# Performance work log

Hardware: AMD Instinct MI355X
Metric: run time of the kernel (lower is better)

Reference implementation:

```python
import jax, jax.numpy as jnp
import numpy as np

BS, H, S, D = 2, 16, 4096, 64
BLOCK = 64
STRIDE_C = 3
NEG = -10000.0


def _global_index(seq_len, block_size, stride_c):
    # static Longformer-style global pattern: first token of each block plus
    # the last `stride_c` tokens of each block
    r = np.arange(seq_len)
    rem = r % block_size
    return np.nonzero((rem == 0) | (rem >= block_size - stride_c))[0]


def setup_inputs() -> dict:
    key = jax.random.key(0)
    k1, k2, k3 = jax.random.split(key, 3)
    q = jax.random.normal(k1, (BS, H, S, D), dtype=jnp.float32)
    k = jax.random.normal(k2, (BS, H, S, D), dtype=jnp.float32)
    v = jax.random.normal(k3, (BS, H, S, D), dtype=jnp.float32)
    mask = jnp.ones((BS, S), dtype=jnp.float32)  # all tokens valid -> pattern is static
    return {"query": q, "key": k, "value": v, "mask": mask}


def reference(query, key, value, mask):
    bs, h, S, d = query.shape
    block = BLOCK
    nb = S // block  # seq_len chosen as multiple of block_size, so pad_len == 0
    g_idx = jnp.asarray(_global_index(S, block, STRIDE_C))  # [G]

    # ---- block-local attention scores ----
    bq = query.reshape(bs, h, nb, block, d)
    bk = key.reshape(bs, h, nb, block, d)
    local = jnp.einsum('bhnxd,bhnyd->bhnxy', bq, bk)  # [bs,h,nb,block,block]
    # additive key-side mask (per key position within each block)
    key_mask = jnp.where(mask == 0.0, NEG, 0.0).reshape(bs, 1, nb, 1, block)
    local = (local + key_mask).reshape(bs, h, S, block)

    # ---- global-token attention scores ----
    gk = key[:, :, g_idx, :]    # [bs,h,G,d]
    gv = value[:, :, g_idx, :]  # [bs,h,G,d]
    gscores = jnp.einsum('bhsd,bhgd->bhsg', query, gk)  # [bs,h,S,G]
    gmask = jnp.where(mask[:, g_idx] == 0.0, NEG, 0.0)[:, None, None, :]
    gscores = gscores + gmask

    # ---- joint softmax over [local block | global tokens] ----
    scores = jnp.concatenate([local, gscores], axis=-1)  # [bs,h,S,block+G]
    probs = jax.nn.softmax(scores.astype(jnp.float32), axis=-1)

    # ---- weighted sums ----
    lp = probs[..., :block].reshape(bs, h, nb, block, block)
    bv = value.reshape(bs, h, nb, block, d)
    lout = jnp.matmul(lp, bv).reshape(bs, h, S, d)
    gout = jnp.einsum('bhsg,bhgd->bhsd', probs[..., block:], gv)
    return lout + gout
```

## Files before the change

kernel.cpp:

```cpp
#include <hip/hip_runtime.h>

#define NEGV -10000.0f

typedef _Float16 f16x8 __attribute__((ext_vector_type(8)));
typedef _Float16 f16x2 __attribute__((ext_vector_type(2)));
typedef float floatx4 __attribute__((ext_vector_type(4)));

__device__ __forceinline__ int src_row(int key, int nblk) {
    if (key < 64) return nblk * 64 + key;
    int g = key - 64;
    int p = g & 3;
    return (g >> 2) * 64 + (p ? (60 + p) : 0);
}

__global__ __launch_bounds__(256, 3)
void sparse_attn_kernel(const float* __restrict__ Q, const float* __restrict__ K,
                        const float* __restrict__ V, const float* __restrict__ M,
                        float* __restrict__ O)
{
    const int x    = blockIdx.x;
    const int bh   = (x & 7) * 4 + ((x >> 3) >> 6);
    const int nblk = (x >> 3) & 63;
    const int b    = bh >> 4;

    const size_t hoff = (size_t)bh * (4096 * 64);
    const float* Qh = Q + hoff;
    const float* Kh = K + hoff;
    const float* Vh = V + hoff;
    float*       Oh = O + hoff;
    const float* Mb = M + (size_t)b * 4096;

    __shared__ _Float16 smem[20480];

    const int tid  = threadIdx.x;
    const int lane = tid & 63;
    const int wv   = tid >> 6;
    const int m    = lane & 15;
    const int quad = lane >> 4;
    const int cg   = tid & 15;
    const int pg   = tid >> 4;

    float mv2[5];
    unsigned long long bb = 0ull;
    #pragma unroll
    for (int s = 0; s < 5; ++s) {
        float mval = Mb[src_row(s * 64 + lane, nblk)];
        bb |= __ballot(mval == 0.0f);
        mv2[s] = (mval == 0.0f) ? NEGV : 0.0f;
    }

    const int qrow = nblk * 64 + wv * 16 + m;
    f16x8 qf[2];
    #pragma unroll
    for (int c = 0; c < 2; ++c) {
        const float* src = Qh + (size_t)qrow * 64 + c * 32 + quad * 8;
        float4 f0 = *(const float4*)src;
        float4 f1 = *(const float4*)(src + 4);
        qf[c][0] = (_Float16)f0.x; qf[c][1] = (_Float16)f0.y;
        qf[c][2] = (_Float16)f0.z; qf[c][3] = (_Float16)f0.w;
        qf[c][4] = (_Float16)f1.x; qf[c][5] = (_Float16)f1.y;
        qf[c][6] = (_Float16)f1.z; qf[c][7] = (_Float16)f1.w;
    }

    #pragma unroll
    for (int it = 0; it < 10; ++it) {
        int S    = it * 256 + tid;
        int t    = S >> 7;
        int n    = S & 15;
        int col0 = ((S >> 6) & 1) * 32 + ((S & 63) >> 4) * 8;
        int lkey = 32 * (t >> 1) + 8 * (n >> 2) + 4 * (t & 1) + (n & 3);
        const float* src = Kh + (size_t)src_row(lkey, nblk) * 64 + col0;
        float4 f0 = *(const float4*)src;
        float4 f1 = *(const float4*)(src + 4);
        f16x8 o;
        o[0] = (_Float16)f0.x; o[1] = (_Float16)f0.y;
        o[2] = (_Float16)f0.z; o[3] = (_Float16)f0.w;
        o[4] = (_Float16)f1.x; o[5] = (_Float16)f1.y;
        o[6] = (_Float16)f1.z; o[7] = (_Float16)f1.w;
        *(f16x8*)(&smem[S * 8]) = o;
    }

    float4 v0a[5], v0b[5];
    #pragma unroll
    for (int it = 0; it < 5; ++it) {
        int l0 = 2 * (it * 16 + pg);
        v0a[it] = *(const float4*)(Vh + (size_t)src_row(l0,     nblk) * 64 + cg * 4);
        v0b[it] = *(const float4*)(Vh + (size_t)src_row(l0 + 1, nblk) * 64 + cg * 4);
    }

    __syncthreads();

    floatx4 acc[20] = {};
    #pragma unroll
    for (int t = 0; t < 20; ++t) {
        #pragma unroll
        for (int c = 0; c < 2; ++c) {
            f16x8 kf = *(const f16x8*)(&smem[(t * 2 + c) * 512 + lane * 8]);
            acc[t] = __builtin_amdgcn_mfma_f32_16x16x32_f16(kf, qf[c], acc[t], 0, 0, 0);
        }
    }

    __syncthreads();

    auto vt_store = [&](int l0, const float4& f0, const float4& f1) {
        int kc2   = l0 >> 5;
        int q2    = (l0 & 31) >> 3;
        int j0    = l0 & 7;
        int td    = cg >> 2;
        int sw    = td << 4;
        int lbase = (kc2 * 4 + td) * 512 + q2 * 128 + (cg & 3) * 32 + j0;
        f16x2 pk0; pk0[0] = (_Float16)f0.x; pk0[1] = (_Float16)f1.x;
        *(f16x2*)(&smem[(lbase +  0) ^ sw]) = pk0;
        f16x2 pk1; pk1[0] = (_Float16)f0.y; pk1[1] = (_Float16)f1.y;
        *(f16x2*)(&smem[(lbase +  8) ^ sw]) = pk1;
        f16x2 pk2; pk2[0] = (_Float16)f0.z; pk2[1] = (_Float16)f1.z;
        *(f16x2*)(&smem[(lbase + 16) ^ sw]) = pk2;
        f16x2 pk3; pk3[0] = (_Float16)f0.w; pk3[1] = (_Float16)f1.w;
        *(f16x2*)(&smem[(lbase + 24) ^ sw]) = pk3;
    };

    #pragma unroll
    for (int it = 0; it < 5; ++it)
        vt_store(2 * (it * 16 + pg), v0a[it], v0b[it]);

    float4 v1a[5], v1b[5];
    #pragma unroll
    for (int it = 0; it < 5; ++it) {
        int l0 = 2 * ((5 + it) * 16 + pg);
        v1a[it] = *(const float4*)(Vh + (size_t)src_row(l0,     nblk) * 64 + cg * 4);
        v1b[it] = *(const float4*)(Vh + (size_t)src_row(l0 + 1, nblk) * 64 + cg * 4);
    }

    if (bb != 0ull) {
        #pragma unroll
        for (int t = 0; t < 20; ++t) {
            int lb = 32 * ((t >> 1) & 1) + 4 * (t & 1) + 8 * quad;
            #pragma unroll
            for (int r = 0; r < 4; ++r)
                acc[t][r] += __shfl(mv2[t >> 2], lb + r, 64);
        }
    }

    float rmax = -3e38f;
    #pragma unroll
    for (int t = 0; t < 20; ++t)
        #pragma unroll
        for (int r = 0; r < 4; ++r)
            rmax = fmaxf(rmax, acc[t][r]);
    rmax = fmaxf(rmax, __shfl_xor(rmax, 16, 64));
    rmax = fmaxf(rmax, __shfl_xor(rmax, 32, 64));
    float rsum = 0.f;
    #pragma unroll
    for (int t = 0; t < 20; ++t)
        #pragma unroll
        for (int r = 0; r < 4; ++r) {
            float e = __expf(acc[t][r] - rmax);
            acc[t][r] = e;
            rsum += e;
        }
    rsum += __shfl_xor(rsum, 16, 64);
    rsum += __shfl_xor(rsum, 32, 64);
    float rinv = 1.0f / rsum;

    #pragma unroll
    for (int it = 0; it < 5; ++it)
        vt_store(2 * ((5 + it) * 16 + pg), v1a[it], v1b[it]);

    f16x8 pf[10];
    #pragma unroll
    for (int k2 = 0; k2 < 10; ++k2) {
        #pragma unroll
        for (int r = 0; r < 4; ++r) {
            pf[k2][r]     = (_Float16)acc[2 * k2][r];
            pf[k2][4 + r] = (_Float16)acc[2 * k2 + 1][r];
        }
    }

    __syncthreads();

    floatx4 oacc[4] = {};
    #pragma unroll
    for (int k2 = 0; k2 < 10; ++k2) {
        #pragma unroll
        for (int t = 0; t < 4; ++t) {
            f16x8 vf = *(const f16x8*)(&smem[(k2 * 4 + t) * 512 + ((lane * 8) ^ (t << 4))]);
            oacc[t] = __builtin_amdgcn_mfma_f32_16x16x32_f16(pf[k2], vf, oacc[t], 0, 0, 0);
        }
    }

    float rinvr[4];
    #pragma unroll
    for (int r = 0; r < 4; ++r)
        rinvr[r] = __shfl(rinv, quad * 4 + r, 64);
    #pragma unroll
    for (int t = 0; t < 4; ++t)
        #pragma unroll
        for (int r = 0; r < 4; ++r)
            Oh[(size_t)(nblk * 64 + wv * 16 + quad * 4 + r) * 64 + t * 16 + m] =
                oacc[t][r] * rinvr[r];
}

extern "C" void kernel_launch(void* const* d_in, const int* in_sizes, int n_in,
                              void* d_out, int out_size, void* d_ws, size_t ws_size,
                              hipStream_t stream) {
    const float* q    = (const float*)d_in[0];
    const float* k    = (const float*)d_in[1];
    const float* v    = (const float*)d_in[2];
    const float* mask = (const float*)d_in[3];
    float* out = (float*)d_out;
    (void)in_sizes; (void)n_in; (void)out_size; (void)d_ws; (void)ws_size;
    sparse_attn_kernel<<<2 * 16 * 64, 256, 0, stream>>>(q, k, v, mask, out);
}
```

Before: 156.8 us.

## Stage V loads in smaller batches to raise occupancy to four blocks per CU

```diff
diff --git a/kernel.cpp b/kernel.cpp
--- a/kernel.cpp
+++ b/kernel.cpp
@@ -13,7 +13,7 @@
     return (g >> 2) * 64 + (p ? (60 + p) : 0);
 }
 
-__global__ __launch_bounds__(256, 3)
+__global__ __launch_bounds__(256, 4)
 void sparse_attn_kernel(const float* __restrict__ Q, const float* __restrict__ K,
                         const float* __restrict__ V, const float* __restrict__ M,
                         float* __restrict__ O)
@@ -80,29 +80,13 @@
         *(f16x8*)(&smem[S * 8]) = o;
     }
 
-    float4 v0a[5], v0b[5];
-    #pragma unroll
-    for (int it = 0; it < 5; ++it) {
+    auto v_load = [&](int it, float4& f0, float4& f1) {
         int l0 = 2 * (it * 16 + pg);
-        v0a[it] = *(const float4*)(Vh + (size_t)src_row(l0,     nblk) * 64 + cg * 4);
-        v0b[it] = *(const float4*)(Vh + (size_t)src_row(l0 + 1, nblk) * 64 + cg * 4);
-    }
-
-    __syncthreads();
-
-    floatx4 acc[20] = {};
-    #pragma unroll
-    for (int t = 0; t < 20; ++t) {
-        #pragma unroll
-        for (int c = 0; c < 2; ++c) {
-            f16x8 kf = *(const f16x8*)(&smem[(t * 2 + c) * 512 + lane * 8]);
-            acc[t] = __builtin_amdgcn_mfma_f32_16x16x32_f16(kf, qf[c], acc[t], 0, 0, 0);
-        }
-    }
-
-    __syncthreads();
-
-    auto vt_store = [&](int l0, const float4& f0, const float4& f1) {
+        f0 = *(const float4*)(Vh + (size_t)src_row(l0,     nblk) * 64 + cg * 4);
+        f1 = *(const float4*)(Vh + (size_t)src_row(l0 + 1, nblk) * 64 + cg * 4);
+    };
+    auto vt_store = [&](int it, const float4& f0, const float4& f1) {
+        int l0    = 2 * (it * 16 + pg);
         int kc2   = l0 >> 5;
         int q2    = (l0 & 31) >> 3;
         int j0    = l0 & 7;
@@ -119,17 +103,32 @@
         *(f16x2*)(&smem[(lbase + 24) ^ sw]) = pk3;
     };
 
-    #pragma unroll
-    for (int it = 0; it < 5; ++it)
-        vt_store(2 * (it * 16 + pg), v0a[it], v0b[it]);
-
-    float4 v1a[5], v1b[5];
-    #pragma unroll
-    for (int it = 0; it < 5; ++it) {
-        int l0 = 2 * ((5 + it) * 16 + pg);
-        v1a[it] = *(const float4*)(Vh + (size_t)src_row(l0,     nblk) * 64 + cg * 4);
-        v1b[it] = *(const float4*)(Vh + (size_t)src_row(l0 + 1, nblk) * 64 + cg * 4);
-    }
+    float4 va0, vb0, va1, vb1, va2, vb2;
+    v_load(0, va0, vb0);
+    v_load(1, va1, vb1);
+    v_load(2, va2, vb2);
+
+    __syncthreads();
+
+    floatx4 acc[20] = {};
+    #pragma unroll
+    for (int t = 0; t < 20; ++t) {
+        #pragma unroll
+        for (int c = 0; c < 2; ++c) {
+            f16x8 kf = *(const f16x8*)(&smem[(t * 2 + c) * 512 + lane * 8]);
+            acc[t] = __builtin_amdgcn_mfma_f32_16x16x32_f16(kf, qf[c], acc[t], 0, 0, 0);
+        }
+    }
+
+    __syncthreads();
+
+    float4 wa0, wb0, wa1, wb1, wa2, wb2;
+    v_load(3, wa0, wb0);
+    v_load(4, wa1, wb1);
+    v_load(5, wa2, wb2);
+    vt_store(0, va0, vb0);
+    vt_store(1, va1, vb1);
+    vt_store(2, va2, vb2);
 
     if (bb != 0ull) {
         #pragma unroll
@@ -149,6 +148,11 @@
             rmax = fmaxf(rmax, acc[t][r]);
     rmax = fmaxf(rmax, __shfl_xor(rmax, 16, 64));
     rmax = fmaxf(rmax, __shfl_xor(rmax, 32, 64));
+
+    vt_store(3, wa0, wb0);
+    vt_store(4, wa1, wb1);
+    vt_store(5, wa2, wb2);
+
     float rsum = 0.f;
     #pragma unroll
     for (int t = 0; t < 20; ++t)
@@ -162,9 +166,9 @@
     rsum += __shfl_xor(rsum, 32, 64);
     float rinv = 1.0f / rsum;
 
-    #pragma unroll
-    for (int it = 0; it < 5; ++it)
-        vt_store(2 * ((5 + it) * 16 + pg), v1a[it], v1b[it]);
+    v_load(6, va0, vb0);
+    v_load(7, va1, vb1);
+    v_load(8, va2, vb2);
 
     f16x8 pf[10];
     #pragma unroll
@@ -175,6 +179,12 @@
             pf[k2][4 + r] = (_Float16)acc[2 * k2 + 1][r];
         }
     }
+
+    vt_store(6, va0, vb0);
+    vt_store(7, va1, vb1);
+    vt_store(8, va2, vb2);
+    v_load(9, wa0, wb0);
+    vt_store(9, wa0, wb0);
 
     __syncthreads();
 
```

New measurement: 170.5 us. +8.8%, slower.

## Load K fragments directly from global into registers, skipping LDS staging

Applied to the files above, without the earlier changes.

```diff
diff --git a/kernel.cpp b/kernel.cpp
--- a/kernel.cpp
+++ b/kernel.cpp
@@ -11,6 +11,15 @@
     int g = key - 64;
     int p = g & 3;
     return (g >> 2) * 64 + (p ? (60 + p) : 0);
+}
+
+__device__ __forceinline__ f16x8 cvt8(const float4& f0, const float4& f1) {
+    f16x8 o;
+    o[0] = (_Float16)f0.x; o[1] = (_Float16)f0.y;
+    o[2] = (_Float16)f0.z; o[3] = (_Float16)f0.w;
+    o[4] = (_Float16)f1.x; o[5] = (_Float16)f1.y;
+    o[6] = (_Float16)f1.z; o[7] = (_Float16)f1.w;
+    return o;
 }
 
 __global__ __launch_bounds__(256, 3)
@@ -56,53 +65,16 @@
         const float* src = Qh + (size_t)qrow * 64 + c * 32 + quad * 8;
         float4 f0 = *(const float4*)src;
         float4 f1 = *(const float4*)(src + 4);
-        qf[c][0] = (_Float16)f0.x; qf[c][1] = (_Float16)f0.y;
-        qf[c][2] = (_Float16)f0.z; qf[c][3] = (_Float16)f0.w;
-        qf[c][4] = (_Float16)f1.x; qf[c][5] = (_Float16)f1.y;
-        qf[c][6] = (_Float16)f1.z; qf[c][7] = (_Float16)f1.w;
-    }
-
-    #pragma unroll
-    for (int it = 0; it < 10; ++it) {
-        int S    = it * 256 + tid;
-        int t    = S >> 7;
-        int n    = S & 15;
-        int col0 = ((S >> 6) & 1) * 32 + ((S & 63) >> 4) * 8;
-        int lkey = 32 * (t >> 1) + 8 * (n >> 2) + 4 * (t & 1) + (n & 3);
-        const float* src = Kh + (size_t)src_row(lkey, nblk) * 64 + col0;
-        float4 f0 = *(const float4*)src;
-        float4 f1 = *(const float4*)(src + 4);
-        f16x8 o;
-        o[0] = (_Float16)f0.x; o[1] = (_Float16)f0.y;
-        o[2] = (_Float16)f0.z; o[3] = (_Float16)f0.w;
-        o[4] = (_Float16)f1.x; o[5] = (_Float16)f1.y;
-        o[6] = (_Float16)f1.z; o[7] = (_Float16)f1.w;
-        *(f16x8*)(&smem[S * 8]) = o;
-    }
-
-    float4 v0a[5], v0b[5];
-    #pragma unroll
-    for (int it = 0; it < 5; ++it) {
+        qf[c] = cvt8(f0, f1);
+    }
+
+    auto v_load = [&](int it, float4& f0, float4& f1) {
         int l0 = 2 * (it * 16 + pg);
-        v0a[it] = *(const float4*)(Vh + (size_t)src_row(l0,     nblk) * 64 + cg * 4);
-        v0b[it] = *(const float4*)(Vh + (size_t)src_row(l0 + 1, nblk) * 64 + cg * 4);
-    }
-
-    __syncthreads();
-
-    floatx4 acc[20] = {};
-    #pragma unroll
-    for (int t = 0; t < 20; ++t) {
-        #pragma unroll
-        for (int c = 0; c < 2; ++c) {
-            f16x8 kf = *(const f16x8*)(&smem[(t * 2 + c) * 512 + lane * 8]);
-            acc[t] = __builtin_amdgcn_mfma_f32_16x16x32_f16(kf, qf[c], acc[t], 0, 0, 0);
-        }
-    }
-
-    __syncthreads();
-
-    auto vt_store = [&](int l0, const float4& f0, const float4& f1) {
+        f0 = *(const float4*)(Vh + (size_t)src_row(l0,     nblk) * 64 + cg * 4);
+        f1 = *(const float4*)(Vh + (size_t)src_row(l0 + 1, nblk) * 64 + cg * 4);
+    };
+    auto vt_store = [&](int it, const float4& f0, const float4& f1) {
+        int l0    = 2 * (it * 16 + pg);
         int kc2   = l0 >> 5;
         int q2    = (l0 & 31) >> 3;
         int j0    = l0 & 7;
@@ -119,17 +91,33 @@
         *(f16x2*)(&smem[(lbase + 24) ^ sw]) = pk3;
     };
 
-    #pragma unroll
-    for (int it = 0; it < 5; ++it)
-        vt_store(2 * (it * 16 + pg), v0a[it], v0b[it]);
-
-    float4 v1a[5], v1b[5];
-    #pragma unroll
-    for (int it = 0; it < 5; ++it) {
-        int l0 = 2 * ((5 + it) * 16 + pg);
-        v1a[it] = *(const float4*)(Vh + (size_t)src_row(l0,     nblk) * 64 + cg * 4);
-        v1b[it] = *(const float4*)(Vh + (size_t)src_row(l0 + 1, nblk) * 64 + cg * 4);
-    }
+    floatx4 acc[20] = {};
+    auto qk_tile = [&](int t) {
+        int lkey = 32 * (t >> 1) + 8 * (m >> 2) + 4 * (t & 1) + (m & 3);
+        const float* src = Kh + (size_t)src_row(lkey, nblk) * 64 + quad * 8;
+        float4 f0 = *(const float4*)src;
+        float4 f1 = *(const float4*)(src + 4);
+        float4 f2 = *(const float4*)(src + 32);
+        float4 f3 = *(const float4*)(src + 36);
+        acc[t] = __builtin_amdgcn_mfma_f32_16x16x32_f16(cvt8(f0, f1), qf[0], acc[t], 0, 0, 0);
+        acc[t] = __builtin_amdgcn_mfma_f32_16x16x32_f16(cvt8(f2, f3), qf[1], acc[t], 0, 0, 0);
+    };
+
+    float4 va[5], vb[5];
+    #pragma unroll
+    for (int it = 0; it < 5; ++it) v_load(it, va[it], vb[it]);
+
+    #pragma unroll
+    for (int t = 0; t < 10; ++t) qk_tile(t);
+
+    #pragma unroll
+    for (int it = 0; it < 5; ++it) vt_store(it, va[it], vb[it]);
+
+    #pragma unroll
+    for (int t = 10; t < 20; ++t) qk_tile(t);
+
+    #pragma unroll
+    for (int it = 0; it < 5; ++it) v_load(5 + it, va[it], vb[it]);
 
     if (bb != 0ull) {
         #pragma unroll
@@ -149,6 +137,10 @@
             rmax = fmaxf(rmax, acc[t][r]);
     rmax = fmaxf(rmax, __shfl_xor(rmax, 16, 64));
     rmax = fmaxf(rmax, __shfl_xor(rmax, 32, 64));
+
+    #pragma unroll
+    for (int it = 0; it < 5; ++it) vt_store(5 + it, va[it], vb[it]);
+
     float rsum = 0.f;
     #pragma unroll
     for (int t = 0; t < 20; ++t)
@@ -161,10 +153,6 @@
     rsum += __shfl_xor(rsum, 16, 64);
     rsum += __shfl_xor(rsum, 32, 64);
     float rinv = 1.0f / rsum;
-
-    #pragma unroll
-    for (int it = 0; it < 5; ++it)
-        vt_store(2 * ((5 + it) * 16 + pg), v1a[it], v1b[it]);
 
     f16x8 pf[10];
     #pragma unroll
```

Result: slower. 202.6 us (+29.3%).

## Split softmax into two online halves to cut registers and raise occupancy

Applied to the files above, without the earlier changes.

```diff
diff --git a/kernel.cpp b/kernel.cpp
--- a/kernel.cpp
+++ b/kernel.cpp
@@ -13,7 +13,16 @@
     return (g >> 2) * 64 + (p ? (60 + p) : 0);
 }
 
-__global__ __launch_bounds__(256, 3)
+__device__ __forceinline__ f16x8 cvt8(const float4& f0, const float4& f1) {
+    f16x8 o;
+    o[0] = (_Float16)f0.x; o[1] = (_Float16)f0.y;
+    o[2] = (_Float16)f0.z; o[3] = (_Float16)f0.w;
+    o[4] = (_Float16)f1.x; o[5] = (_Float16)f1.y;
+    o[6] = (_Float16)f1.z; o[7] = (_Float16)f1.w;
+    return o;
+}
+
+__global__ __launch_bounds__(256, 4)
 void sparse_attn_kernel(const float* __restrict__ Q, const float* __restrict__ K,
                         const float* __restrict__ V, const float* __restrict__ M,
                         float* __restrict__ O)
@@ -56,10 +65,7 @@
         const float* src = Qh + (size_t)qrow * 64 + c * 32 + quad * 8;
         float4 f0 = *(const float4*)src;
         float4 f1 = *(const float4*)(src + 4);
-        qf[c][0] = (_Float16)f0.x; qf[c][1] = (_Float16)f0.y;
-        qf[c][2] = (_Float16)f0.z; qf[c][3] = (_Float16)f0.w;
-        qf[c][4] = (_Float16)f1.x; qf[c][5] = (_Float16)f1.y;
-        qf[c][6] = (_Float16)f1.z; qf[c][7] = (_Float16)f1.w;
+        qf[c] = cvt8(f0, f1);
     }
 
     #pragma unroll
@@ -72,43 +78,21 @@
         const float* src = Kh + (size_t)src_row(lkey, nblk) * 64 + col0;
         float4 f0 = *(const float4*)src;
         float4 f1 = *(const float4*)(src + 4);
-        f16x8 o;
-        o[0] = (_Float16)f0.x; o[1] = (_Float16)f0.y;
-        o[2] = (_Float16)f0.z; o[3] = (_Float16)f0.w;
-        o[4] = (_Float16)f1.x; o[5] = (_Float16)f1.y;
-        o[6] = (_Float16)f1.z; o[7] = (_Float16)f1.w;
-        *(f16x8*)(&smem[S * 8]) = o;
-    }
-
-    float4 v0a[5], v0b[5];
-    #pragma unroll
-    for (int it = 0; it < 5; ++it) {
+        *(f16x8*)(&smem[S * 8]) = cvt8(f0, f1);
+    }
+
+    auto v_load = [&](int it, float4& f0, float4& f1) {
         int l0 = 2 * (it * 16 + pg);
-        v0a[it] = *(const float4*)(Vh + (size_t)src_row(l0,     nblk) * 64 + cg * 4);
-        v0b[it] = *(const float4*)(Vh + (size_t)src_row(l0 + 1, nblk) * 64 + cg * 4);
-    }
-
-    __syncthreads();
-
-    floatx4 acc[20] = {};
-    #pragma unroll
-    for (int t = 0; t < 20; ++t) {
-        #pragma unroll
-        for (int c = 0; c < 2; ++c) {
-            f16x8 kf = *(const f16x8*)(&smem[(t * 2 + c) * 512 + lane * 8]);
-            acc[t] = __builtin_amdgcn_mfma_f32_16x16x32_f16(kf, qf[c], acc[t], 0, 0, 0);
-        }
-    }
-
-    __syncthreads();
-
-    auto vt_store = [&](int l0, const float4& f0, const float4& f1) {
-        int kc2   = l0 >> 5;
-        int q2    = (l0 & 31) >> 3;
-        int j0    = l0 & 7;
+        f0 = *(const float4*)(Vh + (size_t)src_row(l0,     nblk) * 64 + cg * 4);
+        f1 = *(const float4*)(Vh + (size_t)src_row(l0 + 1, nblk) * 64 + cg * 4);
+    };
+    auto vt_store = [&](int it, const float4& f0, const float4& f1) {
+        int itl   = (it < 5) ? it : it - 5;
+        int off   = (it < 5) ? 0 : 10240;
         int td    = cg >> 2;
         int sw    = td << 4;
-        int lbase = (kc2 * 4 + td) * 512 + q2 * 128 + (cg & 3) * 32 + j0;
+        int lbase = off + (itl * 4 + td) * 512 + (pg >> 2) * 128
+                  + (cg & 3) * 32 + 2 * (pg & 3);
         f16x2 pk0; pk0[0] = (_Float16)f0.x; pk0[1] = (_Float16)f1.x;
         *(f16x2*)(&smem[(lbase +  0) ^ sw]) = pk0;
         f16x2 pk1; pk1[0] = (_Float16)f0.y; pk1[1] = (_Float16)f1.y;
@@ -119,85 +103,181 @@
         *(f16x2*)(&smem[(lbase + 24) ^ sw]) = pk3;
     };
 
-    #pragma unroll
-    for (int it = 0; it < 5; ++it)
-        vt_store(2 * (it * 16 + pg), v0a[it], v0b[it]);
-
-    float4 v1a[5], v1b[5];
-    #pragma unroll
-    for (int it = 0; it < 5; ++it) {
-        int l0 = 2 * ((5 + it) * 16 + pg);
-        v1a[it] = *(const float4*)(Vh + (size_t)src_row(l0,     nblk) * 64 + cg * 4);
-        v1b[it] = *(const float4*)(Vh + (size_t)src_row(l0 + 1, nblk) * 64 + cg * 4);
-    }
-
-    if (bb != 0ull) {
-        #pragma unroll
-        for (int t = 0; t < 20; ++t) {
-            int lb = 32 * ((t >> 1) & 1) + 4 * (t & 1) + 8 * quad;
+    floatx4 acc[10];
+    auto mask_add = [&](int tg0) {
+        if (bb != 0ull) {
             #pragma unroll
-            for (int r = 0; r < 4; ++r)
-                acc[t][r] += __shfl(mv2[t >> 2], lb + r, 64);
-        }
-    }
-
-    float rmax = -3e38f;
-    #pragma unroll
-    for (int t = 0; t < 20; ++t)
-        #pragma unroll
-        for (int r = 0; r < 4; ++r)
-            rmax = fmaxf(rmax, acc[t][r]);
-    rmax = fmaxf(rmax, __shfl_xor(rmax, 16, 64));
-    rmax = fmaxf(rmax, __shfl_xor(rmax, 32, 64));
-    float rsum = 0.f;
-    #pragma unroll
-    for (int t = 0; t < 20; ++t)
-        #pragma unroll
-        for (int r = 0; r < 4; ++r) {
-            float e = __expf(acc[t][r] - rmax);
-            acc[t][r] = e;
-            rsum += e;
-        }
-    rsum += __shfl_xor(rsum, 16, 64);
-    rsum += __shfl_xor(rsum, 32, 64);
-    float rinv = 1.0f / rsum;
-
-    #pragma unroll
-    for (int it = 0; it < 5; ++it)
-        vt_store(2 * ((5 + it) * 16 + pg), v1a[it], v1b[it]);
-
-    f16x8 pf[10];
-    #pragma unroll
-    for (int k2 = 0; k2 < 10; ++k2) {
-        #pragma unroll
-        for (int r = 0; r < 4; ++r) {
-            pf[k2][r]     = (_Float16)acc[2 * k2][r];
-            pf[k2][4 + r] = (_Float16)acc[2 * k2 + 1][r];
-        }
-    }
-
-    __syncthreads();
+            for (int tl = 0; tl < 10; ++tl) {
+                int tg = tg0 + tl;
+                int lb = 32 * ((tg >> 1) & 1) + 4 * (tg & 1) + 8 * quad;
+                #pragma unroll
+                for (int r = 0; r < 4; ++r)
+                    acc[tl][r] += __shfl(mv2[tg >> 2], lb + r, 64);
+            }
+        }
+    };
+
+    float4 a0, b0, a1, b1, a2, b2;
+    v_load(0, a0, b0);
+    v_load(1, a1, b1);
+    v_load(2, a2, b2);
+
+    __syncthreads();
+
+    #pragma unroll
+    for (int t = 0; t < 10; ++t) {
+        acc[t] = floatx4{0.f, 0.f, 0.f, 0.f};
+        #pragma unroll
+        for (int c = 0; c < 2; ++c) {
+            f16x8 kf = *(const f16x8*)(&smem[(t * 2 + c) * 512 + lane * 8]);
+            acc[t] = __builtin_amdgcn_mfma_f32_16x16x32_f16(kf, qf[c], acc[t], 0, 0, 0);
+        }
+    }
+
+    __syncthreads();
+
+    vt_store(0, a0, b0);
+    vt_store(1, a1, b1);
+    vt_store(2, a2, b2);
+    v_load(3, a0, b0);
+    v_load(4, a1, b1);
+
+    mask_add(0);
+
+    float m0 = -3e38f;
+    #pragma unroll
+    for (int tl = 0; tl < 10; ++tl)
+        #pragma unroll
+        for (int r = 0; r < 4; ++r)
+            m0 = fmaxf(m0, acc[tl][r]);
+    m0 = fmaxf(m0, __shfl_xor(m0, 16, 64));
+    m0 = fmaxf(m0, __shfl_xor(m0, 32, 64));
+    float s0 = 0.f;
+    #pragma unroll
+    for (int tl = 0; tl < 10; ++tl)
+        #pragma unroll
+        for (int r = 0; r < 4; ++r) {
+            float e = __expf(acc[tl][r] - m0);
+            acc[tl][r] = e;
+            s0 += e;
+        }
+    s0 += __shfl_xor(s0, 16, 64);
+    s0 += __shfl_xor(s0, 32, 64);
+
+    vt_store(3, a0, b0);
+    vt_store(4, a1, b1);
+
+    f16x8 pf0[5];
+    #pragma unroll
+    for (int kc = 0; kc < 5; ++kc)
+        #pragma unroll
+        for (int r = 0; r < 4; ++r) {
+            pf0[kc][r]     = (_Float16)acc[2 * kc][r];
+            pf0[kc][4 + r] = (_Float16)acc[2 * kc + 1][r];
+        }
+
+    __syncthreads();
+
+    v_load(5, a0, b0);
+    v_load(6, a1, b1);
+    v_load(7, a2, b2);
 
     floatx4 oacc[4] = {};
     #pragma unroll
-    for (int k2 = 0; k2 < 10; ++k2) {
+    for (int kc = 0; kc < 5; ++kc) {
         #pragma unroll
         for (int t = 0; t < 4; ++t) {
-            f16x8 vf = *(const f16x8*)(&smem[(k2 * 4 + t) * 512 + ((lane * 8) ^ (t << 4))]);
-            oacc[t] = __builtin_amdgcn_mfma_f32_16x16x32_f16(pf[k2], vf, oacc[t], 0, 0, 0);
-        }
-    }
-
-    float rinvr[4];
+            f16x8 vf = *(const f16x8*)(&smem[(kc * 4 + t) * 512 + ((lane * 8) ^ (t << 4))]);
+            oacc[t] = __builtin_amdgcn_mfma_f32_16x16x32_f16(pf0[kc], vf, oacc[t], 0, 0, 0);
+        }
+    }
+
+    #pragma unroll
+    for (int t = 0; t < 10; ++t) {
+        acc[t] = floatx4{0.f, 0.f, 0.f, 0.f};
+        #pragma unroll
+        for (int c = 0; c < 2; ++c) {
+            f16x8 kf = *(const f16x8*)(&smem[((10 + t) * 2 + c) * 512 + lane * 8]);
+            acc[t] = __builtin_amdgcn_mfma_f32_16x16x32_f16(kf, qf[c], acc[t], 0, 0, 0);
+        }
+    }
+
+    __syncthreads();
+
+    vt_store(5, a0, b0);
+    vt_store(6, a1, b1);
+    vt_store(7, a2, b2);
+    v_load(8, a0, b0);
+    v_load(9, a1, b1);
+
+    mask_add(10);
+
+    float m1 = -3e38f;
+    #pragma unroll
+    for (int tl = 0; tl < 10; ++tl)
+        #pragma unroll
+        for (int r = 0; r < 4; ++r)
+            m1 = fmaxf(m1, acc[tl][r]);
+    m1 = fmaxf(m1, __shfl_xor(m1, 16, 64));
+    m1 = fmaxf(m1, __shfl_xor(m1, 32, 64));
+    const float mg = fmaxf(m0, m1);
+    float s1 = 0.f;
+    #pragma unroll
+    for (int tl = 0; tl < 10; ++tl)
+        #pragma unroll
+        for (int r = 0; r < 4; ++r) {
+            float e = __expf(acc[tl][r] - mg);
+            acc[tl][r] = e;
+            s1 += e;
+        }
+    s1 += __shfl_xor(s1, 16, 64);
+    s1 += __shfl_xor(s1, 32, 64);
+    const float f0   = __expf(m0 - mg);
+    const float zinv = 1.0f / (f0 * s0 + s1);
+
+    float f0r[4];
     #pragma unroll
     for (int r = 0; r < 4; ++r)
-        rinvr[r] = __shfl(rinv, quad * 4 + r, 64);
+        f0r[r] = __shfl(f0, quad * 4 + r, 64);
     #pragma unroll
     for (int t = 0; t < 4; ++t)
         #pragma unroll
         for (int r = 0; r < 4; ++r)
+            oacc[t][r] *= f0r[r];
+
+    vt_store(8, a0, b0);
+    vt_store(9, a1, b1);
+
+    f16x8 pf1[5];
+    #pragma unroll
+    for (int kc = 0; kc < 5; ++kc)
+        #pragma unroll
+        for (int r = 0; r < 4; ++r) {
+            pf1[kc][r]     = (_Float16)acc[2 * kc][r];
+            pf1[kc][4 + r] = (_Float16)acc[2 * kc + 1][r];
+        }
+
+    __syncthreads();
+
+    #pragma unroll
+    for (int kc = 0; kc < 5; ++kc) {
+        #pragma unroll
+        for (int t = 0; t < 4; ++t) {
+            f16x8 vf = *(const f16x8*)(&smem[10240 + (kc * 4 + t) * 512 + ((lane * 8) ^ (t << 4))]);
+            oacc[t] = __builtin_amdgcn_mfma_f32_16x16x32_f16(pf1[kc], vf, oacc[t], 0, 0, 0);
+        }
+    }
+
+    float zr[4];
+    #pragma unroll
+    for (int r = 0; r < 4; ++r)
+        zr[r] = __shfl(zinv, quad * 4 + r, 64);
+    #pragma unroll
+    for (int t = 0; t < 4; ++t)
+        #pragma unroll
+        for (int r = 0; r < 4; ++r)
             Oh[(size_t)(nblk * 64 + wv * 16 + quad * 4 + r) * 64 + t * 16 + m] =
-                oacc[t][r] * rinvr[r];
+                oacc[t][r] * zr[r];
 }
 
 extern "C" void kernel_launch(void* const* d_in, const int* in_sizes, int n_in,
```

Measured after the change: 154.1 us. No clear change (-1.7%).
